# Kernel optimization log

Measured on AMD Instinct MI355X. Metric: run time of the kernel, lower is better.

Reference implementation:

```python
import jax, jax.numpy as jnp
import numpy as np

# Model constants (match init_kwargs)
DIM = 1024
INTER = 1024
E = 32          # n_routed_experts
K = 4           # n_activated_experts
G = 8           # n_expert_groups
LG = 4          # n_limited_groups
ROUTE_SCALE = 1.0
CAP_FACTOR = 1.25
B, S = 4, 2048


def setup_inputs() -> dict:
    key = jax.random.key(0)
    ks = jax.random.split(key, 9)
    sd = DIM ** -0.5
    si = INTER ** -0.5
    x = jax.random.normal(ks[0], (B, S, DIM), jnp.float32)
    wg = jax.random.normal(ks[1], (E, DIM), jnp.float32) * sd          # gate weight [E, dim]
    w1 = jax.random.normal(ks[2], (E, DIM, INTER), jnp.float32) * sd   # stacked expert w1
    w3 = jax.random.normal(ks[3], (E, DIM, INTER), jnp.float32) * sd   # stacked expert w3
    w2 = jax.random.normal(ks[4], (E, INTER, DIM), jnp.float32) * si   # stacked expert w2
    sw1 = jax.random.normal(ks[5], (DIM, INTER), jnp.float32) * sd     # shared SwiGLU
    sw3 = jax.random.normal(ks[6], (DIM, INTER), jnp.float32) * sd
    sw2 = jax.random.normal(ks[7], (INTER, DIM), jnp.float32) * si
    return dict(x=x, wg=wg, w1=w1, w2=w2, w3=w3, sw1=sw1, sw2=sw2, sw3=sw3)


def _gate(xf, wg):
    # Group-limited top-k gating (router_noise_std=0, temperature=1.0).
    logits = xf @ wg.T                                  # [N, E]
    scores = jax.nn.softmax(logits, axis=-1)
    sg = scores.reshape(-1, G, E // G)                  # [N, G, E/G]
    group_scores = sg.max(axis=-1)                      # [N, G]
    _, gtop = jax.lax.top_k(group_scores, LG)           # [N, LG]
    keep_g = jnp.sum(jax.nn.one_hot(gtop, G, dtype=jnp.float32), axis=1) > 0  # [N, G]
    masked = jnp.where(keep_g[:, :, None], sg, -jnp.inf).reshape(-1, E)
    _, idx = jax.lax.top_k(masked, K)                   # [N, K]
    w = jnp.take_along_axis(scores, idx, axis=1)        # gather from ORIGINAL scores
    w = w / (w.sum(-1, keepdims=True) + 1e-9) * ROUTE_SCALE
    return w.astype(xf.dtype), idx


def _forward(x, wg, w1, w2, w3, sw1, sw2, sw3):
    shape = x.shape
    xf = x.reshape(-1, DIM)
    N = xf.shape[0]
    cap = max(1, int(CAP_FACTOR * N * K / E))           # per-expert capacity (static)
    w, idx = _gate(xf, wg)

    # --- dispatch with capacity: position of each (token, slot) within its expert,
    # counted in row-major (token-major) order == torch.where order in the original.
    fe = idx.reshape(-1)                                # [N*K] expert ids
    oh = jax.nn.one_hot(fe, E, dtype=jnp.int32)         # [N*K, E]
    pos = (jnp.cumsum(oh, axis=0) * oh).sum(-1) - 1     # rank within expert
    keep = pos < cap
    dest = jnp.where(keep, fe * cap + pos, E * cap)     # dropped -> pad slot
    tok = jnp.arange(N * K, dtype=jnp.int32) // K
    buf_tok = jnp.full((E * cap + 1,), N, jnp.int32).at[dest].set(tok)[:-1]       # [E*cap]
    buf_w = jnp.zeros((E * cap + 1,), x.dtype).at[dest].set(w.reshape(-1))[:-1]   # [E*cap]

    # --- grouped gather-GEMM-scatter (pad row of zeros for empty slots)
    xp = jnp.concatenate([xf, jnp.zeros((1, DIM), x.dtype)], axis=0)
    xe = xp[buf_tok].reshape(E, cap, DIM)
    h = jax.nn.silu(jnp.einsum('ecd,edh->ech', xe, w1)) * jnp.einsum('ecd,edh->ech', xe, w3)
    out = jnp.einsum('ech,ehd->ecd', h, w2) * buf_w.reshape(E, cap, 1)
    y = jnp.zeros((N + 1, DIM), x.dtype).at[buf_tok].add(out.reshape(E * cap, DIM))[:N]

    # --- shared experts (SwiGLU with inter dim == inter_dim via expansion formula)
    z = (jax.nn.silu(xf @ sw1) * (xf @ sw3)) @ sw2
    return (y + z).reshape(shape)


def reference(x, wg, w1, w2, w3, sw1, sw2, sw3):
    return _forward(x, wg, w1, w2, w3, sw1, sw2, sw3)
```

## Files before the change

### kernel.cpp

```cpp
#include <hip/hip_runtime.h>
#include <stdint.h>

#define NTOK 8192
#define CAP  1280
#define NEXP 32

typedef __bf16 bf16x8 __attribute__((ext_vector_type(8)));
typedef float f32x4 __attribute__((ext_vector_type(4)));
typedef unsigned short u16;

__device__ __forceinline__ u16 f2bf(float f) {
  unsigned u = __builtin_bit_cast(unsigned, f);
  u = (u + 0x7fffu + ((u >> 16) & 1u)) >> 16;
  return (u16)u;
}
__device__ __forceinline__ float bf2f(u16 h) {
  return __builtin_bit_cast(float, ((unsigned)h) << 16);
}

__device__ __forceinline__ void gload16(const void* g, void* l) {
  __builtin_amdgcn_global_load_lds(
      (const __attribute__((address_space(1))) void*)g,
      (__attribute__((address_space(3))) void*)l, 16, 0, 0);
}

__global__ __launch_bounds__(256) void conv_x_kernel(const float* __restrict__ in,
                                                     u16* __restrict__ out) {
  int i = blockIdx.x * 256 + threadIdx.x;
  float4 v = reinterpret_cast<const float4*>(in)[i];
  uint2 o;
  o.x = (unsigned)f2bf(v.x) | ((unsigned)f2bf(v.y) << 16);
  o.y = (unsigned)f2bf(v.z) | ((unsigned)f2bf(v.w) << 16);
  reinterpret_cast<uint2*>(out)[i] = o;
}

__global__ __launch_bounds__(256) void tconv_all_kernel(
    const float* __restrict__ w1, const float* __restrict__ w3,
    const float* __restrict__ w2, const float* __restrict__ sw1,
    const float* __restrict__ sw3, const float* __restrict__ sw2,
    u16* __restrict__ w1t, u16* __restrict__ w3t, u16* __restrict__ w2t,
    u16* __restrict__ sw1t, u16* __restrict__ sw3t, u16* __restrict__ sw2t) {
  __shared__ float tile[32][33];
  const int z = blockIdx.z;
  const float* src;
  u16* dst;
  if (z < 32)      { src = w1 + (size_t)z * 1048576;        dst = w1t + (size_t)z * 1048576; }
  else if (z < 64) { src = w3 + (size_t)(z - 32) * 1048576; dst = w3t + (size_t)(z - 32) * 1048576; }
  else if (z < 96) { src = w2 + (size_t)(z - 64) * 1048576; dst = w2t + (size_t)(z - 64) * 1048576; }
  else if (z == 96){ src = sw1; dst = sw1t; }
  else if (z == 97){ src = sw3; dst = sw3t; }
  else             { src = sw2; dst = sw2t; }
  int r0 = blockIdx.x * 32, c0 = blockIdx.y * 32;
  int tid = threadIdx.x;
#pragma unroll
  for (int i = 0; i < 4; ++i) {
    int t = tid + i * 256, r = t >> 5, c = t & 31;
    tile[r][c] = src[(size_t)(r0 + r) * 1024 + (c0 + c)];
  }
  __syncthreads();
#pragma unroll
  for (int i = 0; i < 4; ++i) {
    int t = tid + i * 256, cc = t >> 5, rr = t & 31;
    dst[(size_t)(c0 + cc) * 1024 + (r0 + rr)] = f2bf(tile[rr][cc]);
  }
}

__global__ __launch_bounds__(256) void gate_kernel(const float* __restrict__ x,
                                                   const float* __restrict__ wg,
                                                   int* __restrict__ gidx,
                                                   float* __restrict__ gw) {
  const int t = blockIdx.x;
  __shared__ float xl[1024];
  __shared__ float logits[32];
  const int tid = threadIdx.x;
  reinterpret_cast<float4*>(xl)[tid] = reinterpret_cast<const float4*>(x + (size_t)t * 1024)[tid];
  __syncthreads();
  const int e = tid >> 3, p = tid & 7;
  const float4* wrow = reinterpret_cast<const float4*>(wg + (size_t)e * 1024);
  const float4* xv4 = reinterpret_cast<const float4*>(xl);
  float s = 0.f;
#pragma unroll
  for (int i = 0; i < 32; ++i) {
    int c = p + 8 * i;
    float4 xv = xv4[c];
    float4 wv = wrow[c];
    s += xv.x * wv.x + xv.y * wv.y + xv.z * wv.z + xv.w * wv.w;
  }
  s += __shfl_xor(s, 1);
  s += __shfl_xor(s, 2);
  s += __shfl_xor(s, 4);
  if (p == 0) logits[e] = s;
  __syncthreads();
  if (tid == 0) {
    float m = logits[0];
#pragma unroll
    for (int i = 1; i < 32; ++i) m = fmaxf(m, logits[i]);
    float sum = 0.f;
#pragma unroll
    for (int i = 0; i < 32; ++i) sum += expf(logits[i] - m);
    float gm[8];
#pragma unroll
    for (int g = 0; g < 8; ++g) {
      float v = logits[4 * g];
      v = fmaxf(v, logits[4 * g + 1]);
      v = fmaxf(v, logits[4 * g + 2]);
      v = fmaxf(v, logits[4 * g + 3]);
      gm[g] = v;
    }
    unsigned gkeep = 0;
    for (int it = 0; it < 4; ++it) {
      float best = -3.4e38f; int bg = 0;
#pragma unroll
      for (int g = 0; g < 8; ++g) {
        bool ok = !((gkeep >> g) & 1u);
        if (ok && gm[g] > best) { best = gm[g]; bg = g; }
      }
      gkeep |= 1u << bg;
    }
    unsigned allow = 0;
#pragma unroll
    for (int g = 0; g < 8; ++g)
      if ((gkeep >> g) & 1u) allow |= 0xFu << (4 * g);
    unsigned taken = 0;
    float wsum = 0.f;
    int ids[4]; float wv[4];
    for (int sIt = 0; sIt < 4; ++sIt) {
      float best = -3.4e38f; int be = 0;
#pragma unroll
      for (int i = 0; i < 32; ++i) {
        bool ok = ((allow >> i) & 1u) && !((taken >> i) & 1u);
        float v = logits[i];
        if (ok && v > best) { best = v; be = i; }
      }
      taken |= 1u << be;
      ids[sIt] = be;
      float wq = expf(logits[be] - m) / sum;
      wv[sIt] = wq;
      wsum += wq;
    }
    float inv = 1.f / (wsum + 1e-9f);
#pragma unroll
    for (int sIt = 0; sIt < 4; ++sIt) {
      gidx[t * 4 + sIt] = ids[sIt];
      gw[t * 4 + sIt] = wv[sIt] * inv;
    }
  }
}

__global__ __launch_bounds__(256) void initbuf_kernel(int* __restrict__ bt, float* __restrict__ bw) {
  int i = blockIdx.x * 256 + threadIdx.x;
  if (i < NEXP * CAP) { bt[i] = -1; bw[i] = 0.f; }
}

__global__ __launch_bounds__(1024) void rank_kernel(const int* __restrict__ gidx,
                                                    const float* __restrict__ gw,
                                                    int* __restrict__ buf_tok,
                                                    float* __restrict__ buf_w,
                                                    int* __restrict__ cnt,
                                                    int* __restrict__ tslot) {
  const int e = blockIdx.x;
  const int tid = threadIdx.x, wid = tid >> 6, lane = tid & 63;
  __shared__ int wtot[16];
  int base = 0;
  for (int j0 = 0; j0 < NTOK * 4; j0 += 1024) {
    int j = j0 + tid;
    bool match = (gidx[j] == e);
    unsigned long long mb = __ballot(match);
    if (lane == 0) wtot[wid] = __popcll(mb);
    __syncthreads();
    int woff = 0, btot = 0;
#pragma unroll
    for (int w = 0; w < 16; ++w) {
      int c = wtot[w];
      if (w < wid) woff += c;
      btot += c;
    }
    if (match) {
      int pos = base + woff + __popcll(mb & ((1ull << lane) - 1ull));
      if (pos < CAP) {
        buf_tok[e * CAP + pos] = j >> 2;
        buf_w[e * CAP + pos] = gw[j];
        tslot[j] = e * CAP + pos;
      } else {
        tslot[j] = -1;
      }
    }
    base += btot;
    __syncthreads();
  }
  if (tid == 0) cnt[e] = (base < CAP) ? base : CAP;
}

#define UPPH(S, STAGE_EXPR, WAIT_STMT)                                           \
  {                                                                              \
    const u16* aB = aRd + (S) * 16384;                                           \
    const u16* bB = bRd + (S) * 16384;                                           \
    bf16x8 av[8], bv[4];                                                         \
    _Pragma("unroll") for (int m = 0; m < 8; ++m)                                \
        av[m] = *reinterpret_cast<const bf16x8*>(aB + m * 512);                  \
    _Pragma("unroll") for (int n = 0; n < 4; ++n)                                \
        bv[n] = *reinterpret_cast<const bf16x8*>(bB + n * 512);                  \
    STAGE_EXPR;                                                                  \
    WAIT_STMT;                                                                   \
    __builtin_amdgcn_s_barrier();                                                \
    __builtin_amdgcn_s_setprio(1);                                               \
    _Pragma("unroll") for (int m = 0; m < 8; ++m)                                \
      _Pragma("unroll") for (int n = 0; n < 4; ++n)                              \
        acc[m][n] = __builtin_amdgcn_mfma_f32_16x16x32_bf16(av[m], bv[n],        \
                                                            acc[m][n], 0, 0, 0);\
    __builtin_amdgcn_s_setprio(0);                                               \
    __builtin_amdgcn_s_barrier();                                                \
  }

#define VM8 asm volatile("s_waitcnt vmcnt(8)" ::: "memory")
#define VM4 asm volatile("s_waitcnt vmcnt(4)" ::: "memory")
#define VM0 asm volatile("s_waitcnt vmcnt(0)" ::: "memory")

__global__ __launch_bounds__(512) void up8_kernel(const u16* __restrict__ X,
                                                  const u16* __restrict__ w1t,
                                                  const u16* __restrict__ w3t,
                                                  const u16* __restrict__ sw1t,
                                                  const u16* __restrict__ sw3t,
                                                  u16* __restrict__ hs,
                                                  u16* __restrict__ he,
                                                  const int* __restrict__ btok,
                                                  const int* __restrict__ cnt) {
  extern __shared__ __align__(16) u16 lds_raw[];
  const int tid = threadIdx.x, wid = tid >> 6, lane = tid & 63;
  const int bid = blockIdx.x;
  const int xcd = bid & 7, off = bid >> 3;
  bool expert;
  int mt, nt, e = 0;
  const u16 *B1, *B3;
  u16* H;
  if (off < 160) {
    expert = true;
    int id = xcd * 160 + off;
    e = id / 40;
    int r = id % 40;
    mt = r % 5;
    nt = r / 5;
    if (mt * 256 >= cnt[e]) return;
    B1 = w1t + ((size_t)e << 20);
    B3 = w3t + ((size_t)e << 20);
    H = he + (size_t)(e * CAP + mt * 256) * 1024;
  } else {
    expert = false;
    int id = xcd * 32 + (off - 160);
    mt = id % 32;
    nt = id / 32;
    B1 = sw1t;
    B3 = sw3t;
    H = hs + (size_t)mt * 256 * 1024;
  }
  const int wr = wid >> 2, wc = wid & 3;
  const int fr = lane & 15, fw = lane >> 4;

  const int srow = tid >> 2;
  const int slot = tid & 3;
  const int sw = ((slot ^ ((srow >> 1) & 3)) << 3);

  const u16* aP[2];
#pragma unroll
  for (int j = 0; j < 2; ++j) {
    int row = mt * 256 + j * 128 + srow;
    int grow;
    if (expert) {
      int t0 = btok[e * CAP + row];
      grow = (t0 < 0) ? 0 : t0;
    } else {
      grow = row;
    }
    aP[j] = X + (size_t)grow * 1024 + sw;
  }
  const u16* bP[2];
  bP[0] = B1 + (size_t)(nt * 128 + srow) * 1024 + sw;
  bP[1] = B3 + (size_t)(nt * 128 + srow) * 1024 + sw;

  const int sdst = wid * 512;

  auto stage = [&](int c) {
    u16* dA = lds_raw + (c & 3) * 16384 + sdst;
    u16* dB = dA + 8192;
    const int g = c * 32;
    gload16(aP[0] + g, dA);
    gload16(aP[1] + g, dA + 4096);
    gload16(bP[0] + g, dB);
    gload16(bP[1] + g, dB + 4096);
  };

  const int swz = ((fw ^ ((fr >> 1) & 3)) << 3);
  const u16* aRd = lds_raw + (wr * 128 + fr) * 32 + swz;
  const u16* bRd = lds_raw + 8192 + (wc * 64 + fr) * 32 + swz;

  f32x4 acc[8][4] = {};

  stage(0);
  stage(1);
  stage(2);
  VM8;
  __builtin_amdgcn_s_barrier();

  for (int t = 0; t < 7; ++t) {
    const int p0 = t * 4;
    UPPH(0, stage(p0 + 3), VM8)
    UPPH(1, stage(p0 + 4), VM8)
    UPPH(2, stage(p0 + 5), VM8)
    UPPH(3, stage(p0 + 6), VM8)
  }
  UPPH(0, stage(31), VM8)
  UPPH(1, (void)0, VM4)
  UPPH(2, (void)0, VM0)
  UPPH(3, (void)0, (void)0)

  float* lf = reinterpret_cast<float*>(lds_raw);
  if (wc >= 2) {
    float* dst = lf + (wr * 2 + (wc - 2)) * 8192 + lane;
#pragma unroll
    for (int m = 0; m < 8; ++m)
#pragma unroll
      for (int n = 0; n < 4; ++n)
#pragma unroll
        for (int ri = 0; ri < 4; ++ri)
          dst[(m * 16 + n * 4 + ri) * 64] = acc[m][n][ri];
  }
  __syncthreads();
  if (wc < 2) {
    const float* src = lf + (wr * 2 + wc) * 8192 + lane;
    const int row0 = wr * 128 + fw * 4;
    const int col0 = nt * 128 + wc * 64;
#pragma unroll
    for (int m = 0; m < 8; ++m)
#pragma unroll
      for (int n = 0; n < 4; ++n)
#pragma unroll
        for (int ri = 0; ri < 4; ++ri) {
          float v1 = acc[m][n][ri];
          float v3 = src[(m * 16 + n * 4 + ri) * 64];
          float h = (v1 / (1.f + __expf(-v1))) * v3;
          H[(size_t)(row0 + m * 16 + ri) * 1024 + col0 + n * 16 + fr] = f2bf(h);
        }
  }
}

__global__ __launch_bounds__(512) void down8_kernel(const u16* __restrict__ hs,
                                                    const u16* __restrict__ he,
                                                    const u16* __restrict__ sB,
                                                    const u16* __restrict__ eB,
                                                    float* __restrict__ Out,
                                                    u16* __restrict__ OutB,
                                                    const float* __restrict__ bw,
                                                    const int* __restrict__ cnt) {
  extern __shared__ __align__(16) u16 lds_raw[];
  const int tid = threadIdx.x, wid = tid >> 6, lane = tid & 63;
  const int bid = blockIdx.x;
  const int xcd = bid & 7, off = bid >> 3;
  bool expert;
  int mt, nt, e = 0;
  const u16 *Asrc, *Bsrc;
  if (off < 80) {
    expert = true;
    int id = xcd * 80 + off;
    e = id / 20;
    int r = id % 20;
    mt = r % 5;
    nt = r / 5;
    if (mt * 256 >= cnt[e]) return;
    Asrc = he + (size_t)e * CAP * 1024;
    Bsrc = eB + ((size_t)e << 20);
  } else {
    expert = false;
    int id = xcd * 16 + (off - 80);
    mt = id % 32;
    nt = id / 32;
    Asrc = hs;
    Bsrc = sB;
  }
  const int wr = wid >> 2, wc = wid & 3;

  const int srow = wid * 8 + (lane >> 3);
  const int sslot = lane & 7;
  const int swin = ((sslot ^ (srow & 7)) << 3);
  const u16* aS = Asrc + (size_t)(mt * 256 + srow) * 1024 + swin;
  const u16* bS = Bsrc + (size_t)(nt * 256 + srow) * 1024 + swin;

  auto ldsA = [&](int b) { return lds_raw + b * 32768; };
  auto ldsB = [&](int b) { return lds_raw + b * 32768 + 16384; };

  auto stageA = [&](int b, int kt) {
    u16* base = ldsA(b);
#pragma unroll
    for (int j = 0; j < 4; ++j)
      gload16(aS + (size_t)j * 64 * 1024 + kt * 64, base + (j * 64 + wid * 8) * 64);
  };
  auto stageB = [&](int b, int kt) {
    u16* base = ldsB(b);
#pragma unroll
    for (int j = 0; j < 4; ++j)
      gload16(bS + (size_t)j * 64 * 1024 + kt * 64, base + (j * 64 + wid * 8) * 64);
  };

  const int fr = lane & 15, fw = lane >> 4;
  auto Afrag = [&](int cur, int m, int ks) -> bf16x8 {
    int r = wr * 128 + m * 16 + fr;
    int W = ks * 4 + fw;
    return *reinterpret_cast<const bf16x8*>(ldsA(cur) + r * 64 + ((W ^ (r & 7)) << 3));
  };
  auto Bfrag = [&](int cur, int n, int ks) -> bf16x8 {
    int r = wc * 64 + n * 16 + fr;
    int W = ks * 4 + fw;
    return *reinterpret_cast<const bf16x8*>(ldsB(cur) + r * 64 + ((W ^ (r & 7)) << 3));
  };

  f32x4 acc[8][4] = {};

  stageA(0, 0);
  stageB(0, 0);
  asm volatile("s_waitcnt vmcnt(0)" ::: "memory");
  __builtin_amdgcn_s_barrier();

  for (int kt = 0; kt < 16; ++kt) {
    const int cur = kt & 1;
    const bool pf = (kt + 1 < 16);
    bf16x8 bfr[4][2];
#pragma unroll
    for (int n = 0; n < 4; ++n) {
      bfr[n][0] = Bfrag(cur, n, 0);
      bfr[n][1] = Bfrag(cur, n, 1);
    }
    {
      bf16x8 a00 = Afrag(cur, 0, 0), a01 = Afrag(cur, 0, 1);
      bf16x8 a10 = Afrag(cur, 1, 0), a11 = Afrag(cur, 1, 1);
      if (pf) stageA(cur ^ 1, kt + 1);
      __builtin_amdgcn_s_barrier();
      __builtin_amdgcn_s_setprio(1);
#pragma unroll
      for (int n = 0; n < 4; ++n) {
        acc[0][n] = __builtin_amdgcn_mfma_f32_16x16x32_bf16(a00, bfr[n][0], acc[0][n], 0, 0, 0);
        acc[0][n] = __builtin_amdgcn_mfma_f32_16x16x32_bf16(a01, bfr[n][1], acc[0][n], 0, 0, 0);
        acc[1][n] = __builtin_amdgcn_mfma_f32_16x16x32_bf16(a10, bfr[n][0], acc[1][n], 0, 0, 0);
        acc[1][n] = __builtin_amdgcn_mfma_f32_16x16x32_bf16(a11, bfr[n][1], acc[1][n], 0, 0, 0);
      }
      __builtin_amdgcn_s_setprio(0);
      __builtin_amdgcn_s_barrier();
    }
    {
      bf16x8 a00 = Afrag(cur, 2, 0), a01 = Afrag(cur, 2, 1);
      bf16x8 a10 = Afrag(cur, 3, 0), a11 = Afrag(cur, 3, 1);
      if (pf) stageB(cur ^ 1, kt + 1);
      __builtin_amdgcn_s_barrier();
      __builtin_amdgcn_s_setprio(1);
#pragma unroll
      for (int n = 0; n < 4; ++n) {
        acc[2][n] = __builtin_amdgcn_mfma_f32_16x16x32_bf16(a00, bfr[n][0], acc[2][n], 0, 0, 0);
        acc[2][n] = __builtin_amdgcn_mfma_f32_16x16x32_bf16(a01, bfr[n][1], acc[2][n], 0, 0, 0);
        acc[3][n] = __builtin_amdgcn_mfma_f32_16x16x32_bf16(a10, bfr[n][0], acc[3][n], 0, 0, 0);
        acc[3][n] = __builtin_amdgcn_mfma_f32_16x16x32_bf16(a11, bfr[n][1], acc[3][n], 0, 0, 0);
      }
      __builtin_amdgcn_s_setprio(0);
      __builtin_amdgcn_s_barrier();
    }
    {
      bf16x8 a00 = Afrag(cur, 4, 0), a01 = Afrag(cur, 4, 1);
      bf16x8 a10 = Afrag(cur, 5, 0), a11 = Afrag(cur, 5, 1);
      __builtin_amdgcn_s_barrier();
      __builtin_amdgcn_s_setprio(1);
#pragma unroll
      for (int n = 0; n < 4; ++n) {
        acc[4][n] = __builtin_amdgcn_mfma_f32_16x16x32_bf16(a00, bfr[n][0], acc[4][n], 0, 0, 0);
        acc[4][n] = __builtin_amdgcn_mfma_f32_16x16x32_bf16(a01, bfr[n][1], acc[4][n], 0, 0, 0);
        acc[5][n] = __builtin_amdgcn_mfma_f32_16x16x32_bf16(a10, bfr[n][0], acc[5][n], 0, 0, 0);
        acc[5][n] = __builtin_amdgcn_mfma_f32_16x16x32_bf16(a11, bfr[n][1], acc[5][n], 0, 0, 0);
      }
      __builtin_amdgcn_s_setprio(0);
      __builtin_amdgcn_s_barrier();
    }
    {
      bf16x8 a00 = Afrag(cur, 6, 0), a01 = Afrag(cur, 6, 1);
      bf16x8 a10 = Afrag(cur, 7, 0), a11 = Afrag(cur, 7, 1);
      __builtin_amdgcn_s_barrier();
      __builtin_amdgcn_s_setprio(1);
#pragma unroll
      for (int n = 0; n < 4; ++n) {
        acc[6][n] = __builtin_amdgcn_mfma_f32_16x16x32_bf16(a00, bfr[n][0], acc[6][n], 0, 0, 0);
        acc[6][n] = __builtin_amdgcn_mfma_f32_16x16x32_bf16(a01, bfr[n][1], acc[6][n], 0, 0, 0);
        acc[7][n] = __builtin_amdgcn_mfma_f32_16x16x32_bf16(a10, bfr[n][0], acc[7][n], 0, 0, 0);
        acc[7][n] = __builtin_amdgcn_mfma_f32_16x16x32_bf16(a11, bfr[n][1], acc[7][n], 0, 0, 0);
      }
      __builtin_amdgcn_s_setprio(0);
      asm volatile("s_waitcnt vmcnt(0)" ::: "memory");
      __builtin_amdgcn_s_barrier();
    }
  }

  const int orow0 = mt * 256 + wr * 128 + fw * 4;
  const int ocol0 = nt * 256 + wc * 64;
  if (expert) {
#pragma unroll
    for (int m = 0; m < 8; ++m)
#pragma unroll
      for (int ri = 0; ri < 4; ++ri) {
        int row = orow0 + m * 16 + ri;
        int slot = e * CAP + row;
        float wgt = bw[slot];
#pragma unroll
        for (int n = 0; n < 4; ++n)
          OutB[(size_t)slot * 1024 + ocol0 + n * 16 + fr] = f2bf(acc[m][n][ri] * wgt);
      }
  } else {
#pragma unroll
    for (int m = 0; m < 8; ++m)
#pragma unroll
      for (int ri = 0; ri < 4; ++ri) {
        int row = orow0 + m * 16 + ri;
#pragma unroll
        for (int n = 0; n < 4; ++n)
          Out[(size_t)row * 1024 + ocol0 + n * 16 + fr] = acc[m][n][ri];
      }
  }
}

__global__ __launch_bounds__(256) void combine_kernel(const u16* __restrict__ oe,
                                                      const int* __restrict__ tslot,
                                                      float* __restrict__ out) {
  const int t = blockIdx.x;
  const int c = threadIdx.x;
  int s0 = tslot[t * 4 + 0], s1 = tslot[t * 4 + 1];
  int s2 = tslot[t * 4 + 2], s3 = tslot[t * 4 + 3];
  float4 v = reinterpret_cast<float4*>(out + (size_t)t * 1024)[c];
  auto addsl = [&](int s) {
    if (s >= 0) {
      uint2 q = reinterpret_cast<const uint2*>(oe + (size_t)s * 1024)[c];
      v.x += bf2f((u16)(q.x & 0xffff));
      v.y += bf2f((u16)(q.x >> 16));
      v.z += bf2f((u16)(q.y & 0xffff));
      v.w += bf2f((u16)(q.y >> 16));
    }
  };
  addsl(s0); addsl(s1); addsl(s2); addsl(s3);
  reinterpret_cast<float4*>(out + (size_t)t * 1024)[c] = v;
}

extern "C" void kernel_launch(void* const* d_in, const int* in_sizes, int n_in,
                              void* d_out, int out_size, void* d_ws, size_t ws_size,
                              hipStream_t stream) {
  const float* x   = (const float*)d_in[0];
  const float* wg  = (const float*)d_in[1];
  const float* w1  = (const float*)d_in[2];
  const float* w2  = (const float*)d_in[3];
  const float* w3  = (const float*)d_in[4];
  const float* sw1 = (const float*)d_in[5];
  const float* sw2 = (const float*)d_in[6];
  const float* sw3 = (const float*)d_in[7];
  float* out = (float*)d_out;

  char* p = (char*)d_ws;
  auto alloc = [&](size_t bytes) {
    char* q = p;
    p += (bytes + 255) & ~(size_t)255;
    return q;
  };
  u16* xb   = (u16*)alloc((size_t)NTOK * 1024 * 2);
  u16* w1t  = (u16*)alloc((size_t)NEXP * 1024 * 1024 * 2);
  u16* w3t  = (u16*)alloc((size_t)NEXP * 1024 * 1024 * 2);
  u16* w2t  = (u16*)alloc((size_t)NEXP * 1024 * 1024 * 2);
  u16* sw1t = (u16*)alloc((size_t)1024 * 1024 * 2);
  u16* sw3t = (u16*)alloc((size_t)1024 * 1024 * 2);
  u16* sw2t = (u16*)alloc((size_t)1024 * 1024 * 2);
  u16* hs   = (u16*)alloc((size_t)NTOK * 1024 * 2);
  u16* he   = (u16*)alloc((size_t)NEXP * CAP * 1024 * 2);
  int*   gidx = (int*)alloc((size_t)NTOK * 4 * 4);
  float* gww  = (float*)alloc((size_t)NTOK * 4 * 4);
  int*   btok = (int*)alloc((size_t)NEXP * CAP * 4);
  float* bww  = (float*)alloc((size_t)NEXP * CAP * 4);
  int*   cnt  = (int*)alloc((size_t)NEXP * 4);
  int*   tslot= (int*)alloc((size_t)NTOK * 4 * 4);
  u16* oe = w1t;

  conv_x_kernel<<<NTOK * 1024 / 1024, 256, 0, stream>>>(x, xb);
  tconv_all_kernel<<<dim3(32, 32, 99), 256, 0, stream>>>(w1, w3, w2, sw1, sw3, sw2,
                                                         w1t, w3t, w2t, sw1t, sw3t, sw2t);
  gate_kernel<<<NTOK, 256, 0, stream>>>(x, wg, gidx, gww);
  initbuf_kernel<<<(NEXP * CAP + 255) / 256, 256, 0, stream>>>(btok, bww);
  rank_kernel<<<NEXP, 1024, 0, stream>>>(gidx, gww, btok, bww, cnt, tslot);
  up8_kernel<<<1536, 512, 131072, stream>>>(xb, w1t, w3t, sw1t, sw3t, hs, he, btok, cnt);
  down8_kernel<<<768, 512, 131072, stream>>>(hs, he, sw2t, w2t, out, oe, bww, cnt);
  combine_kernel<<<NTOK, 256, 0, stream>>>(oe, tslot, out);
}
```

Before: 580.9 us.

## Shrink MoE GEMM tiles and LDS to raise occupancy with double buffering

Both the up-projection and down-projection grouped GEMMs move from 256x256-style tiles with 4-stage (up) or large double-buffered (down) LDS pipelines to smaller tiles (256x64 interleaved w1/w3 for up, 256x128 for down) with a simple 2-stage LDS buffer of 48KB. Launch bounds now request 4 waves per SIMD and grid sizes double. The up kernel interleaves w1 and w3 rows in the B tile, so SiLU*gate is computed in registers without the LDS exchange. The aim is more resident blocks per CU to hide latency. The cost is less data reuse per tile and a full vmcnt(0) wait plus barrier every K step.

```diff
diff --git a/kernel.cpp b/kernel.cpp
--- a/kernel.cpp
+++ b/kernel.cpp
@@ -23,6 +23,8 @@
       (const __attribute__((address_space(1))) void*)g,
       (__attribute__((address_space(3))) void*)l, 16, 0, 0);
 }
+
+#define VM0 asm volatile("s_waitcnt vmcnt(0)" ::: "memory")
 
 __global__ __launch_bounds__(256) void conv_x_kernel(const float* __restrict__ in,
                                                      u16* __restrict__ out) {
@@ -191,40 +193,15 @@
   if (tid == 0) cnt[e] = (base < CAP) ? base : CAP;
 }
 
-#define UPPH(S, STAGE_EXPR, WAIT_STMT)                                           \
-  {                                                                              \
-    const u16* aB = aRd + (S) * 16384;                                           \
-    const u16* bB = bRd + (S) * 16384;                                           \
-    bf16x8 av[8], bv[4];                                                         \
-    _Pragma("unroll") for (int m = 0; m < 8; ++m)                                \
-        av[m] = *reinterpret_cast<const bf16x8*>(aB + m * 512);                  \
-    _Pragma("unroll") for (int n = 0; n < 4; ++n)                                \
-        bv[n] = *reinterpret_cast<const bf16x8*>(bB + n * 512);                  \
-    STAGE_EXPR;                                                                  \
-    WAIT_STMT;                                                                   \
-    __builtin_amdgcn_s_barrier();                                                \
-    __builtin_amdgcn_s_setprio(1);                                               \
-    _Pragma("unroll") for (int m = 0; m < 8; ++m)                                \
-      _Pragma("unroll") for (int n = 0; n < 4; ++n)                              \
-        acc[m][n] = __builtin_amdgcn_mfma_f32_16x16x32_bf16(av[m], bv[n],        \
-                                                            acc[m][n], 0, 0, 0);\
-    __builtin_amdgcn_s_setprio(0);                                               \
-    __builtin_amdgcn_s_barrier();                                                \
-  }
-
-#define VM8 asm volatile("s_waitcnt vmcnt(8)" ::: "memory")
-#define VM4 asm volatile("s_waitcnt vmcnt(4)" ::: "memory")
-#define VM0 asm volatile("s_waitcnt vmcnt(0)" ::: "memory")
-
-__global__ __launch_bounds__(512) void up8_kernel(const u16* __restrict__ X,
-                                                  const u16* __restrict__ w1t,
-                                                  const u16* __restrict__ w3t,
-                                                  const u16* __restrict__ sw1t,
-                                                  const u16* __restrict__ sw3t,
-                                                  u16* __restrict__ hs,
-                                                  u16* __restrict__ he,
-                                                  const int* __restrict__ btok,
-                                                  const int* __restrict__ cnt) {
+__global__ __launch_bounds__(512, 4) void up8_kernel(const u16* __restrict__ X,
+                                                     const u16* __restrict__ w1t,
+                                                     const u16* __restrict__ w3t,
+                                                     const u16* __restrict__ sw1t,
+                                                     const u16* __restrict__ sw3t,
+                                                     u16* __restrict__ hs,
+                                                     u16* __restrict__ he,
+                                                     const int* __restrict__ btok,
+                                                     const int* __restrict__ cnt) {
   extern __shared__ __align__(16) u16 lds_raw[];
   const int tid = threadIdx.x, wid = tid >> 6, lane = tid & 63;
   const int bid = blockIdx.x;
@@ -233,6 +210,124 @@
   int mt, nt, e = 0;
   const u16 *B1, *B3;
   u16* H;
+  if (off < 320) {
+    expert = true;
+    int id = xcd * 320 + off;
+    e = id / 80;
+    int r = id % 80;
+    mt = r % 5;
+    nt = r / 5;
+    if (mt * 256 >= cnt[e]) return;
+    B1 = w1t + ((size_t)e << 20);
+    B3 = w3t + ((size_t)e << 20);
+    H = he + (size_t)(e * CAP + mt * 256) * 1024;
+  } else {
+    expert = false;
+    int id = xcd * 64 + (off - 320);
+    mt = id % 32;
+    nt = id / 32;
+    B1 = sw1t;
+    B3 = sw3t;
+    H = hs + (size_t)mt * 256 * 1024;
+  }
+  const int wr = wid >> 1, wc = wid & 1;
+  const int fr = lane & 15, fw = lane >> 4;
+
+  const int srow = tid >> 2;
+  const int slot4 = tid & 3;
+  const int sw = ((slot4 ^ ((srow >> 1) & 3)) << 3);
+
+  const u16* aP[2];
+#pragma unroll
+  for (int j = 0; j < 2; ++j) {
+    int row = mt * 256 + j * 128 + srow;
+    int grow;
+    if (expert) {
+      int t0 = btok[e * CAP + row];
+      grow = (t0 < 0) ? 0 : t0;
+    } else {
+      grow = row;
+    }
+    aP[j] = X + (size_t)grow * 1024 + sw;
+  }
+  const u16* bP;
+  {
+    int q = srow >> 5, s = srow & 31;
+    const u16* base = (s < 16) ? B1 : B3;
+    bP = base + (size_t)(nt * 64 + q * 16 + (s & 15)) * 1024 + sw;
+  }
+
+  auto stage = [&](int c) {
+    u16* dA = lds_raw + (c & 1) * 12288 + wid * 512;
+    const int g = c * 32;
+    gload16(aP[0] + g, dA);
+    gload16(aP[1] + g, dA + 4096);
+    gload16(bP + g, dA + 8192);
+  };
+
+  const int swz = ((fw ^ ((fr >> 1) & 3)) << 3);
+  const u16* aRd = lds_raw + (wr * 64 + fr) * 32 + swz;
+  const u16* bRd = lds_raw + 8192 + (wc * 64 + fr) * 32 + swz;
+
+  f32x4 acc[4][4] = {};
+
+  stage(0);
+  VM0;
+  __builtin_amdgcn_s_barrier();
+
+  for (int c = 0; c < 32; ++c) {
+    const int off16 = (c & 1) * 12288;
+    bf16x8 av[4], bv[4];
+#pragma unroll
+    for (int m = 0; m < 4; ++m)
+      av[m] = *reinterpret_cast<const bf16x8*>(aRd + off16 + m * 512);
+#pragma unroll
+    for (int n = 0; n < 4; ++n)
+      bv[n] = *reinterpret_cast<const bf16x8*>(bRd + off16 + n * 512);
+    if (c < 31) stage(c + 1);
+    __builtin_amdgcn_s_setprio(1);
+#pragma unroll
+    for (int m = 0; m < 4; ++m)
+#pragma unroll
+      for (int n = 0; n < 4; ++n)
+        acc[m][n] = __builtin_amdgcn_mfma_f32_16x16x32_bf16(av[m], bv[n], acc[m][n], 0, 0, 0);
+    __builtin_amdgcn_s_setprio(0);
+    if (c < 31) {
+      VM0;
+      __builtin_amdgcn_s_barrier();
+    }
+  }
+
+  const int row0 = wr * 64 + fw * 4;
+  const int col0 = nt * 64 + wc * 32;
+#pragma unroll
+  for (int m = 0; m < 4; ++m)
+#pragma unroll
+    for (int k = 0; k < 2; ++k)
+#pragma unroll
+      for (int ri = 0; ri < 4; ++ri) {
+        float v1 = acc[m][2 * k][ri];
+        float v3 = acc[m][2 * k + 1][ri];
+        float h = (v1 / (1.f + __expf(-v1))) * v3;
+        H[(size_t)(row0 + m * 16 + ri) * 1024 + col0 + k * 16 + fr] = f2bf(h);
+      }
+}
+
+__global__ __launch_bounds__(512, 4) void down8_kernel(const u16* __restrict__ hs,
+                                                       const u16* __restrict__ he,
+                                                       const u16* __restrict__ sB,
+                                                       const u16* __restrict__ eB,
+                                                       float* __restrict__ Out,
+                                                       u16* __restrict__ OutB,
+                                                       const float* __restrict__ bw,
+                                                       const int* __restrict__ cnt) {
+  extern __shared__ __align__(16) u16 lds_raw[];
+  const int tid = threadIdx.x, wid = tid >> 6, lane = tid & 63;
+  const int bid = blockIdx.x;
+  const int xcd = bid & 7, off = bid >> 3;
+  bool expert;
+  int mt, nt, e = 0;
+  const u16 *Asrc, *Bsrc;
   if (off < 160) {
     expert = true;
     int id = xcd * 160 + off;
@@ -241,275 +336,88 @@
     mt = r % 5;
     nt = r / 5;
     if (mt * 256 >= cnt[e]) return;
-    B1 = w1t + ((size_t)e << 20);
-    B3 = w3t + ((size_t)e << 20);
-    H = he + (size_t)(e * CAP + mt * 256) * 1024;
+    Asrc = he + (size_t)e * CAP * 1024;
+    Bsrc = eB + ((size_t)e << 20);
   } else {
     expert = false;
     int id = xcd * 32 + (off - 160);
     mt = id % 32;
     nt = id / 32;
-    B1 = sw1t;
-    B3 = sw3t;
-    H = hs + (size_t)mt * 256 * 1024;
-  }
-  const int wr = wid >> 2, wc = wid & 3;
+    Asrc = hs;
+    Bsrc = sB;
+  }
+  const int wr = wid >> 1, wc = wid & 1;
   const int fr = lane & 15, fw = lane >> 4;
 
   const int srow = tid >> 2;
-  const int slot = tid & 3;
-  const int sw = ((slot ^ ((srow >> 1) & 3)) << 3);
+  const int slot4 = tid & 3;
+  const int sw = ((slot4 ^ ((srow >> 1) & 3)) << 3);
 
   const u16* aP[2];
 #pragma unroll
-  for (int j = 0; j < 2; ++j) {
-    int row = mt * 256 + j * 128 + srow;
-    int grow;
-    if (expert) {
-      int t0 = btok[e * CAP + row];
-      grow = (t0 < 0) ? 0 : t0;
-    } else {
-      grow = row;
-    }
-    aP[j] = X + (size_t)grow * 1024 + sw;
-  }
-  const u16* bP[2];
-  bP[0] = B1 + (size_t)(nt * 128 + srow) * 1024 + sw;
-  bP[1] = B3 + (size_t)(nt * 128 + srow) * 1024 + sw;
-
-  const int sdst = wid * 512;
+  for (int j = 0; j < 2; ++j)
+    aP[j] = Asrc + (size_t)(mt * 256 + j * 128 + srow) * 1024 + sw;
+  const u16* bP = Bsrc + (size_t)(nt * 128 + srow) * 1024 + sw;
 
   auto stage = [&](int c) {
-    u16* dA = lds_raw + (c & 3) * 16384 + sdst;
-    u16* dB = dA + 8192;
+    u16* dA = lds_raw + (c & 1) * 12288 + wid * 512;
     const int g = c * 32;
     gload16(aP[0] + g, dA);
     gload16(aP[1] + g, dA + 4096);
-    gload16(bP[0] + g, dB);
-    gload16(bP[1] + g, dB + 4096);
+    gload16(bP + g, dA + 8192);
   };
 
   const int swz = ((fw ^ ((fr >> 1) & 3)) << 3);
-  const u16* aRd = lds_raw + (wr * 128 + fr) * 32 + swz;
+  const u16* aRd = lds_raw + (wr * 64 + fr) * 32 + swz;
   const u16* bRd = lds_raw + 8192 + (wc * 64 + fr) * 32 + swz;
 
-  f32x4 acc[8][4] = {};
+  f32x4 acc[4][4] = {};
 
   stage(0);
-  stage(1);
-  stage(2);
-  VM8;
+  VM0;
   __builtin_amdgcn_s_barrier();
 
-  for (int t = 0; t < 7; ++t) {
-    const int p0 = t * 4;
-    UPPH(0, stage(p0 + 3), VM8)
-    UPPH(1, stage(p0 + 4), VM8)
-    UPPH(2, stage(p0 + 5), VM8)
-    UPPH(3, stage(p0 + 6), VM8)
-  }
-  UPPH(0, stage(31), VM8)
-  UPPH(1, (void)0, VM4)
-  UPPH(2, (void)0, VM0)
-  UPPH(3, (void)0, (void)0)
-
-  float* lf = reinterpret_cast<float*>(lds_raw);
-  if (wc >= 2) {
-    float* dst = lf + (wr * 2 + (wc - 2)) * 8192 + lane;
-#pragma unroll
-    for (int m = 0; m < 8; ++m)
+  for (int c = 0; c < 32; ++c) {
+    const int off16 = (c & 1) * 12288;
+    bf16x8 av[4], bv[4];
+#pragma unroll
+    for (int m = 0; m < 4; ++m)
+      av[m] = *reinterpret_cast<const bf16x8*>(aRd + off16 + m * 512);
+#pragma unroll
+    for (int n = 0; n < 4; ++n)
+      bv[n] = *reinterpret_cast<const bf16x8*>(bRd + off16 + n * 512);
+    if (c < 31) stage(c + 1);
+    __builtin_amdgcn_s_setprio(1);
+#pragma unroll
+    for (int m = 0; m < 4; ++m)
 #pragma unroll
       for (int n = 0; n < 4; ++n)
-#pragma unroll
-        for (int ri = 0; ri < 4; ++ri)
-          dst[(m * 16 + n * 4 + ri) * 64] = acc[m][n][ri];
-  }
-  __syncthreads();
-  if (wc < 2) {
-    const float* src = lf + (wr * 2 + wc) * 8192 + lane;
-    const int row0 = wr * 128 + fw * 4;
-    const int col0 = nt * 128 + wc * 64;
-#pragma unroll
-    for (int m = 0; m < 8; ++m)
-#pragma unroll
-      for (int n = 0; n < 4; ++n)
-#pragma unroll
-        for (int ri = 0; ri < 4; ++ri) {
-          float v1 = acc[m][n][ri];
-          float v3 = src[(m * 16 + n * 4 + ri) * 64];
-          float h = (v1 / (1.f + __expf(-v1))) * v3;
-          H[(size_t)(row0 + m * 16 + ri) * 1024 + col0 + n * 16 + fr] = f2bf(h);
-        }
-  }
-}
-
-__global__ __launch_bounds__(512) void down8_kernel(const u16* __restrict__ hs,
-                                                    const u16* __restrict__ he,
-                                                    const u16* __restrict__ sB,
-                                                    const u16* __restrict__ eB,
-                                                    float* __restrict__ Out,
-                                                    u16* __restrict__ OutB,
-                                                    const float* __restrict__ bw,
-                                                    const int* __restrict__ cnt) {
-  extern __shared__ __align__(16) u16 lds_raw[];
-  const int tid = threadIdx.x, wid = tid >> 6, lane = tid & 63;
-  const int bid = blockIdx.x;
-  const int xcd = bid & 7, off = bid >> 3;
-  bool expert;
-  int mt, nt, e = 0;
-  const u16 *Asrc, *Bsrc;
-  if (off < 80) {
-    expert = true;
-    int id = xcd * 80 + off;
-    e = id / 20;
-    int r = id % 20;
-    mt = r % 5;
-    nt = r / 5;
-    if (mt * 256 >= cnt[e]) return;
-    Asrc = he + (size_t)e * CAP * 1024;
-    Bsrc = eB + ((size_t)e << 20);
-  } else {
-    expert = false;
-    int id = xcd * 16 + (off - 80);
-    mt = id % 32;
-    nt = id / 32;
-    Asrc = hs;
-    Bsrc = sB;
-  }
-  const int wr = wid >> 2, wc = wid & 3;
-
-  const int srow = wid * 8 + (lane >> 3);
-  const int sslot = lane & 7;
-  const int swin = ((sslot ^ (srow & 7)) << 3);
-  const u16* aS = Asrc + (size_t)(mt * 256 + srow) * 1024 + swin;
-  const u16* bS = Bsrc + (size_t)(nt * 256 + srow) * 1024 + swin;
-
-  auto ldsA = [&](int b) { return lds_raw + b * 32768; };
-  auto ldsB = [&](int b) { return lds_raw + b * 32768 + 16384; };
-
-  auto stageA = [&](int b, int kt) {
-    u16* base = ldsA(b);
-#pragma unroll
-    for (int j = 0; j < 4; ++j)
-      gload16(aS + (size_t)j * 64 * 1024 + kt * 64, base + (j * 64 + wid * 8) * 64);
-  };
-  auto stageB = [&](int b, int kt) {
-    u16* base = ldsB(b);
-#pragma unroll
-    for (int j = 0; j < 4; ++j)
-      gload16(bS + (size_t)j * 64 * 1024 + kt * 64, base + (j * 64 + wid * 8) * 64);
-  };
-
-  const int fr = lane & 15, fw = lane >> 4;
-  auto Afrag = [&](int cur, int m, int ks) -> bf16x8 {
-    int r = wr * 128 + m * 16 + fr;
-    int W = ks * 4 + fw;
-    return *reinterpret_cast<const bf16x8*>(ldsA(cur) + r * 64 + ((W ^ (r & 7)) << 3));
-  };
-  auto Bfrag = [&](int cur, int n, int ks) -> bf16x8 {
-    int r = wc * 64 + n * 16 + fr;
-    int W = ks * 4 + fw;
-    return *reinterpret_cast<const bf16x8*>(ldsB(cur) + r * 64 + ((W ^ (r & 7)) << 3));
-  };
-
-  f32x4 acc[8][4] = {};
-
-  stageA(0, 0);
-  stageB(0, 0);
-  asm volatile("s_waitcnt vmcnt(0)" ::: "memory");
-  __builtin_amdgcn_s_barrier();
-
-  for (int kt = 0; kt < 16; ++kt) {
-    const int cur = kt & 1;
-    const bool pf = (kt + 1 < 16);
-    bf16x8 bfr[4][2];
-#pragma unroll
-    for (int n = 0; n < 4; ++n) {
-      bfr[n][0] = Bfrag(cur, n, 0);
-      bfr[n][1] = Bfrag(cur, n, 1);
-    }
-    {
-      bf16x8 a00 = Afrag(cur, 0, 0), a01 = Afrag(cur, 0, 1);
-      bf16x8 a10 = Afrag(cur, 1, 0), a11 = Afrag(cur, 1, 1);
-      if (pf) stageA(cur ^ 1, kt + 1);
+        acc[m][n] = __builtin_amdgcn_mfma_f32_16x16x32_bf16(av[m], bv[n], acc[m][n], 0, 0, 0);
+    __builtin_amdgcn_s_setprio(0);
+    if (c < 31) {
+      VM0;
       __builtin_amdgcn_s_barrier();
-      __builtin_amdgcn_s_setprio(1);
-#pragma unroll
-      for (int n = 0; n < 4; ++n) {
-        acc[0][n] = __builtin_amdgcn_mfma_f32_16x16x32_bf16(a00, bfr[n][0], acc[0][n], 0, 0, 0);
-        acc[0][n] = __builtin_amdgcn_mfma_f32_16x16x32_bf16(a01, bfr[n][1], acc[0][n], 0, 0, 0);
-        acc[1][n] = __builtin_amdgcn_mfma_f32_16x16x32_bf16(a10, bfr[n][0], acc[1][n], 0, 0, 0);
-        acc[1][n] = __builtin_amdgcn_mfma_f32_16x16x32_bf16(a11, bfr[n][1], acc[1][n], 0, 0, 0);
-      }
-      __builtin_amdgcn_s_setprio(0);
-      __builtin_amdgcn_s_barrier();
-    }
-    {
-      bf16x8 a00 = Afrag(cur, 2, 0), a01 = Afrag(cur, 2, 1);
-      bf16x8 a10 = Afrag(cur, 3, 0), a11 = Afrag(cur, 3, 1);
-      if (pf) stageB(cur ^ 1, kt + 1);
-      __builtin_amdgcn_s_barrier();
-      __builtin_amdgcn_s_setprio(1);
-#pragma unroll
-      for (int n = 0; n < 4; ++n) {
-        acc[2][n] = __builtin_amdgcn_mfma_f32_16x16x32_bf16(a00, bfr[n][0], acc[2][n], 0, 0, 0);
-        acc[2][n] = __builtin_amdgcn_mfma_f32_16x16x32_bf16(a01, bfr[n][1], acc[2][n], 0, 0, 0);
-        acc[3][n] = __builtin_amdgcn_mfma_f32_16x16x32_bf16(a10, bfr[n][0], acc[3][n], 0, 0, 0);
-        acc[3][n] = __builtin_amdgcn_mfma_f32_16x16x32_bf16(a11, bfr[n][1], acc[3][n], 0, 0, 0);
-      }
-      __builtin_amdgcn_s_setprio(0);
-      __builtin_amdgcn_s_barrier();
-    }
-    {
-      bf16x8 a00 = Afrag(cur, 4, 0), a01 = Afrag(cur, 4, 1);
-      bf16x8 a10 = Afrag(cur, 5, 0), a11 = Afrag(cur, 5, 1);
-      __builtin_amdgcn_s_barrier();
-      __builtin_amdgcn_s_setprio(1);
-#pragma unroll
-      for (int n = 0; n < 4; ++n) {
-        acc[4][n] = __builtin_amdgcn_mfma_f32_16x16x32_bf16(a00, bfr[n][0], acc[4][n], 0, 0, 0);
-        acc[4][n] = __builtin_amdgcn_mfma_f32_16x16x32_bf16(a01, bfr[n][1], acc[4][n], 0, 0, 0);
-        acc[5][n] = __builtin_amdgcn_mfma_f32_16x16x32_bf16(a10, bfr[n][0], acc[5][n], 0, 0, 0);
-        acc[5][n] = __builtin_amdgcn_mfma_f32_16x16x32_bf16(a11, bfr[n][1], acc[5][n], 0, 0, 0);
-      }
-      __builtin_amdgcn_s_setprio(0);
-      __builtin_amdgcn_s_barrier();
-    }
-    {
-      bf16x8 a00 = Afrag(cur, 6, 0), a01 = Afrag(cur, 6, 1);
-      bf16x8 a10 = Afrag(cur, 7, 0), a11 = Afrag(cur, 7, 1);
-      __builtin_amdgcn_s_barrier();
-      __builtin_amdgcn_s_setprio(1);
-#pragma unroll
-      for (int n = 0; n < 4; ++n) {
-        acc[6][n] = __builtin_amdgcn_mfma_f32_16x16x32_bf16(a00, bfr[n][0], acc[6][n], 0, 0, 0);
-        acc[6][n] = __builtin_amdgcn_mfma_f32_16x16x32_bf16(a01, bfr[n][1], acc[6][n], 0, 0, 0);
-        acc[7][n] = __builtin_amdgcn_mfma_f32_16x16x32_bf16(a10, bfr[n][0], acc[7][n], 0, 0, 0);
-        acc[7][n] = __builtin_amdgcn_mfma_f32_16x16x32_bf16(a11, bfr[n][1], acc[7][n], 0, 0, 0);
-      }
-      __builtin_amdgcn_s_setprio(0);
-      asm volatile("s_waitcnt vmcnt(0)" ::: "memory");
-      __builtin_amdgcn_s_barrier();
-    }
-  }
-
-  const int orow0 = mt * 256 + wr * 128 + fw * 4;
-  const int ocol0 = nt * 256 + wc * 64;
+    }
+  }
+
+  const int orow0 = mt * 256 + wr * 64 + fw * 4;
+  const int ocol0 = nt * 128 + wc * 64;
   if (expert) {
 #pragma unroll
-    for (int m = 0; m < 8; ++m)
+    for (int m = 0; m < 4; ++m)
 #pragma unroll
       for (int ri = 0; ri < 4; ++ri) {
         int row = orow0 + m * 16 + ri;
-        int slot = e * CAP + row;
-        float wgt = bw[slot];
+        int slot = e * CAP + (row - mt * 256) + mt * 256;
+        float wgt = bw[e * CAP + row];
 #pragma unroll
         for (int n = 0; n < 4; ++n)
-          OutB[(size_t)slot * 1024 + ocol0 + n * 16 + fr] = f2bf(acc[m][n][ri] * wgt);
+          OutB[(size_t)(e * CAP + row) * 1024 + ocol0 + n * 16 + fr] = f2bf(acc[m][n][ri] * wgt);
+        (void)slot;
       }
   } else {
 #pragma unroll
-    for (int m = 0; m < 8; ++m)
+    for (int m = 0; m < 4; ++m)
 #pragma unroll
       for (int ri = 0; ri < 4; ++ri) {
         int row = orow0 + m * 16 + ri;
@@ -583,7 +491,7 @@
   gate_kernel<<<NTOK, 256, 0, stream>>>(x, wg, gidx, gww);
   initbuf_kernel<<<(NEXP * CAP + 255) / 256, 256, 0, stream>>>(btok, bww);
   rank_kernel<<<NEXP, 1024, 0, stream>>>(gidx, gww, btok, bww, cnt, tslot);
-  up8_kernel<<<1536, 512, 131072, stream>>>(xb, w1t, w3t, sw1t, sw3t, hs, he, btok, cnt);
-  down8_kernel<<<768, 512, 131072, stream>>>(hs, he, sw2t, w2t, out, oe, bww, cnt);
+  up8_kernel<<<3072, 512, 49152, stream>>>(xb, w1t, w3t, sw1t, sw3t, hs, he, btok, cnt);
+  down8_kernel<<<1536, 512, 49152, stream>>>(hs, he, sw2t, w2t, out, oe, bww, cnt);
   combine_kernel<<<NTOK, 256, 0, stream>>>(oe, tslot, out);
 }
```

After: 578.2 us. No clear change (-0.5%).
